# Kernel optimization log

Measured on AMD Instinct MI355X. Metric: run time of the kernel, lower is better.

Reference implementation:

```python
import jax, jax.numpy as jnp
from jax import lax
import numpy as np

B, C, L = 8, 64, 32768
K = 4
DEPTH = 8


def _causal_depthwise_conv(x, weight, dilation):
    # x: [B, C, L], weight: [C, 1, K] depthwise (groups=C). stride=1 so the
    # torch pad formula reduces to left-pad dilation*(K-1), output length L.
    pad = dilation * (K - 1)
    return lax.conv_general_dilated(
        x, weight,
        window_strides=(1,),
        padding=[(pad, 0)],
        rhs_dilation=(dilation,),
        dimension_numbers=("NCH", "OIH", "NCH"),
        feature_group_count=C,
    )


def setup_inputs() -> dict:
    key = jax.random.key(0)
    k1, k2, k3, k4 = jax.random.split(key, 4)
    scalar = np.sqrt(2.0 / (K * 2)).astype(np.float32)
    w_scale = np.sqrt(2.0 / (2 * DEPTH + 4)).astype(np.float32)
    return {
        "x": jax.random.normal(k1, (B, C, L), dtype=jnp.float32),
        "h0": jax.random.uniform(k2, (C, 1, K), minval=-1.0, maxval=1.0, dtype=jnp.float32) * scalar,
        "h1": jax.random.uniform(k3, (C, 1, K), minval=-1.0, maxval=1.0, dtype=jnp.float32) * scalar,
        "w": jax.random.uniform(k4, (C, DEPTH + 2), minval=-1.0, maxval=1.0, dtype=jnp.float32) * w_scale,
    }


def reference(x, h0, h1, w):
    residual_low = x
    y = jnp.zeros_like(x)
    dilation = 1
    for i in range(DEPTH, 0, -1):
        residual_high = _causal_depthwise_conv(residual_low, h1, dilation)
        residual_low = _causal_depthwise_conv(residual_low, h0, dilation)
        y = y + w[:, i][None, :, None] * residual_high
        dilation *= 2
    y = y + w[:, 0][None, :, None] * residual_low
    y = y + x * w[:, -1][None, :, None]
    # dropout p=0 is identity; torch GELU default is exact (erf)
    return jax.nn.gelu(y, approximate=False)
```

## Files before the change

### kernel.cpp

```cpp
#include <hip/hip_runtime.h>
#include <cmath>

namespace {

typedef _Float16 h8 __attribute__((ext_vector_type(8)));

constexpr int C_     = 64;
constexpr int L_     = 32768;
constexpr int TILE   = 4096;
constexpr int HALO   = 776;
constexpr int NB     = TILE + HALO;
constexpr int NU     = NB / 8;
constexpr int HALO_U = HALO / 8;
constexpr int NT     = L_ / TILE;
constexpr int BLK    = 256;
constexpr int UMAX   = (NU + BLK - 1) / BLK;

__device__ __forceinline__ h8 ld8(const _Float16* p) { return *reinterpret_cast<const h8*>(p); }
__device__ __forceinline__ void st8(_Float16* p, h8 v) { *reinterpret_cast<h8*>(p) = v; }
__device__ __forceinline__ float4 ld4f(const float* p) { return *reinterpret_cast<const float4*>(p); }
__device__ __forceinline__ void st4f(float* p, float4 v) { *reinterpret_cast<float4*>(p) = v; }
__device__ __forceinline__ h8 sp8(_Float16 v) { return (h8){v,v,v,v,v,v,v,v}; }

__device__ __forceinline__ h8 fma8(h8 a, h8 b, h8 c) {
    return __builtin_elementwise_fma(a, b, c);
}

template<int K>
__device__ __forceinline__ h8 shconc(h8 A, h8 B) {
    return __builtin_shufflevector(A, B, K, K+1, K+2, K+3, K+4, K+5, K+6, K+7);
}

__device__ __forceinline__ float gelu_f(float v) {
    const float z = v * (1.5957691216057308f + 0.0713548162726f * v * v);
    const float e = __expf(-z);
    return v * __builtin_amdgcn_rcpf(1.0f + e);
}

template<int D, int STARTU, bool LAST>
__device__ __forceinline__ void level_pass(const _Float16* __restrict__ src,
                                           _Float16* __restrict__ dst,
                                           const float* h0f, const float* h1f,
                                           float wi, float w0,
                                           h8* lw, h8* yacc, int tid)
{
    _Float16 c1[4], c0[4];
#pragma unroll
    for (int t = 0; t < 4; ++t) {
        c1[t] = (_Float16)(wi * h1f[t]);
        c0[t] = (_Float16)(LAST ? w0 * h0f[t] : h0f[t]);
    }

#pragma unroll
    for (int u = 0; u < UMAX; ++u) {
        const int un = tid + u * BLK;
        if (un >= STARTU && un < NU) {
            const int p = 8 * un;
            const h8 T3 = lw[u];
            h8 T0, T1, T2;
            if constexpr (D == 1) {
                h8 Lv = ld8(&src[p - 8]);
                T0 = shconc<5>(Lv, T3);
                T1 = shconc<6>(Lv, T3);
                T2 = shconc<7>(Lv, T3);
            } else if constexpr (D == 2) {
                h8 Lv = ld8(&src[p - 8]);
                T0 = shconc<2>(Lv, T3);
                T1 = shconc<4>(Lv, T3);
                T2 = shconc<6>(Lv, T3);
            } else if constexpr (D == 4) {
                h8 Lv  = ld8(&src[p - 8]);
                h8 LL  = ld8(&src[p - 16]);
                T0 = shconc<4>(LL, Lv);
                T1 = Lv;
                T2 = shconc<4>(Lv, T3);
            } else {
                T0 = ld8(&src[p - 3 * D]);
                T1 = ld8(&src[p - 2 * D]);
                T2 = ld8(&src[p - D]);
            }
            if (un >= HALO_U) {
                h8 yv = yacc[u];
                yv = fma8(sp8(c1[0]), T0, yv);
                yv = fma8(sp8(c1[1]), T1, yv);
                yv = fma8(sp8(c1[2]), T2, yv);
                yv = fma8(sp8(c1[3]), T3, yv);
                yacc[u] = yv;
            }
            h8 nl = sp8(c0[0]) * T0;
            nl = fma8(sp8(c0[1]), T1, nl);
            nl = fma8(sp8(c0[2]), T2, nl);
            nl = fma8(sp8(c0[3]), T3, nl);
            if constexpr (LAST) {
                yacc[u] += nl;
            } else {
                lw[u] = nl;
                st8(&dst[p], nl);
            }
        }
    }
}

__global__ __launch_bounds__(BLK, 8)
void cmrc_kernel(const float* __restrict__ x,
                 const float* __restrict__ h0,
                 const float* __restrict__ h1,
                 const float* __restrict__ w,
                 float* __restrict__ out)
{
    __shared__ alignas(16) _Float16 buf[2][NB];

    const int tid  = threadIdx.x;
    const int blk  = blockIdx.x;
    const int tile = blk % NT;
    const int bc   = blk / NT;
    const int c    = bc % C_;
    const long row = (long)bc * L_;
    const int  t0  = tile * TILE - HALO;

    float h0v[4], h1v[4];
#pragma unroll
    for (int k = 0; k < 4; ++k) { h0v[k] = h0[c*4+k]; h1v[k] = h1[c*4+k]; }
    float wv[10];
#pragma unroll
    for (int i = 0; i < 10; ++i) wv[i] = w[c*10+i];

    h8 lw[UMAX];
    h8 yacc[UMAX];

    const _Float16 w9h = (_Float16)wv[9];

#pragma unroll
    for (int u = 0; u < UMAX; ++u) {
        yacc[u] = sp8((_Float16)0.f);
        const int un = tid + u * BLK;
        if (un < NU) {
            const int p = 8 * un;
            const int t = t0 + p;
            float4 xa = make_float4(0.f, 0.f, 0.f, 0.f);
            float4 xb = make_float4(0.f, 0.f, 0.f, 0.f);
            if (t >= 0)     xa = ld4f(&x[row + t]);
            if (t + 4 >= 0) xb = ld4f(&x[row + t + 4]);
            h8 hv;
            hv[0] = (_Float16)xa.x; hv[1] = (_Float16)xa.y;
            hv[2] = (_Float16)xa.z; hv[3] = (_Float16)xa.w;
            hv[4] = (_Float16)xb.x; hv[5] = (_Float16)xb.y;
            hv[6] = (_Float16)xb.z; hv[7] = (_Float16)xb.w;
            st8(&buf[0][p], hv);
            lw[u] = hv;
            if (un >= HALO_U) yacc[u] = sp8(w9h) * hv;
        }
    }
    __syncthreads();

    level_pass<1,   1,  false>(buf[0], buf[1], h0v, h1v, wv[8], 0.f, lw, yacc, tid); __syncthreads();
    level_pass<2,   2,  false>(buf[1], buf[0], h0v, h1v, wv[7], 0.f, lw, yacc, tid); __syncthreads();
    level_pass<4,   4,  false>(buf[0], buf[1], h0v, h1v, wv[6], 0.f, lw, yacc, tid); __syncthreads();
    level_pass<8,   7,  false>(buf[1], buf[0], h0v, h1v, wv[5], 0.f, lw, yacc, tid); __syncthreads();
    level_pass<16,  13, false>(buf[0], buf[1], h0v, h1v, wv[4], 0.f, lw, yacc, tid); __syncthreads();
    level_pass<32,  25, false>(buf[1], buf[0], h0v, h1v, wv[3], 0.f, lw, yacc, tid); __syncthreads();
    level_pass<64,  49, false>(buf[0], buf[1], h0v, h1v, wv[2], 0.f, lw, yacc, tid); __syncthreads();
    level_pass<128, 97, true >(buf[1], buf[0], h0v, h1v, wv[1], wv[0], lw, yacc, tid);

#pragma unroll
    for (int u = 0; u < UMAX; ++u) {
        const int un = tid + u * BLK;
        if (un >= HALO_U && un < NU) {
            const int p = 8 * un;
            const h8 v = yacc[u];
            float4 oa, ob;
            oa.x = gelu_f((float)v[0]); oa.y = gelu_f((float)v[1]);
            oa.z = gelu_f((float)v[2]); oa.w = gelu_f((float)v[3]);
            ob.x = gelu_f((float)v[4]); ob.y = gelu_f((float)v[5]);
            ob.z = gelu_f((float)v[6]); ob.w = gelu_f((float)v[7]);
            st4f(&out[row + t0 + p], oa);
            st4f(&out[row + t0 + p + 4], ob);
        }
    }
}

}

extern "C" void kernel_launch(void* const* d_in, const int* in_sizes, int n_in,
                              void* d_out, int out_size, void* d_ws, size_t ws_size,
                              hipStream_t stream)
{
    const float* x  = (const float*)d_in[0];
    const float* h0 = (const float*)d_in[1];
    const float* h1 = (const float*)d_in[2];
    const float* w  = (const float*)d_in[3];
    float* out = (float*)d_out;

    const int nblocks = (out_size / L_) * NT;
    cmrc_kernel<<<nblocks, BLK, 0, stream>>>(x, h0, h1, w, out);
}
```

Measured before the change: 43.26 us.

## Double tile and block size to cut halo recompute, specialize unit loop, pack via cvt_pkrtz

```diff
diff --git a/kernel.cpp b/kernel.cpp
--- a/kernel.cpp
+++ b/kernel.cpp
@@ -4,17 +4,20 @@
 namespace {
 
 typedef _Float16 h8 __attribute__((ext_vector_type(8)));
+typedef _Float16 h2 __attribute__((ext_vector_type(2)));
+typedef __fp16   fp2 __attribute__((ext_vector_type(2)));
+typedef _Float16 h4 __attribute__((ext_vector_type(4)));
 
 constexpr int C_     = 64;
 constexpr int L_     = 32768;
-constexpr int TILE   = 4096;
+constexpr int TILE   = 8192;
 constexpr int HALO   = 776;
 constexpr int NB     = TILE + HALO;
 constexpr int NU     = NB / 8;
 constexpr int HALO_U = HALO / 8;
 constexpr int NT     = L_ / TILE;
-constexpr int BLK    = 256;
-constexpr int UMAX   = (NU + BLK - 1) / BLK;
+constexpr int BLK    = 512;
+constexpr int S2N    = NU - 2 * BLK;
 
 __device__ __forceinline__ h8 ld8(const _Float16* p) { return *reinterpret_cast<const h8*>(p); }
 __device__ __forceinline__ void st8(_Float16* p, h8 v) { *reinterpret_cast<h8*>(p) = v; }
@@ -31,10 +34,60 @@
     return __builtin_shufflevector(A, B, K, K+1, K+2, K+3, K+4, K+5, K+6, K+7);
 }
 
+__device__ __forceinline__ h2 pkrtz(float lo, float hi) {
+    const fp2 r = __builtin_amdgcn_cvt_pkrtz(lo, hi);
+    return __builtin_bit_cast(h2, r);
+}
+__device__ __forceinline__ h8 pack8(float4 a, float4 b) {
+    const h2 p0 = pkrtz(a.x, a.y);
+    const h2 p1 = pkrtz(a.z, a.w);
+    const h2 p2 = pkrtz(b.x, b.y);
+    const h2 p3 = pkrtz(b.z, b.w);
+    return (h8){p0[0], p0[1], p1[0], p1[1], p2[0], p2[1], p3[0], p3[1]};
+}
+
 __device__ __forceinline__ float gelu_f(float v) {
     const float z = v * (1.5957691216057308f + 0.0713548162726f * v * v);
     const float e = __expf(-z);
     return v * __builtin_amdgcn_rcpf(1.0f + e);
+}
+
+template<int D, bool LAST>
+__device__ __forceinline__ void unit_math(const _Float16* __restrict__ src,
+                                          int p, h8& lwv, h8& yv, bool doY,
+                                          const _Float16* c1, const _Float16* c0)
+{
+    const h8 T3 = lwv;
+    h8 T0, T1, T2;
+    if constexpr (D == 1) {
+        const h8 Lv = ld8(&src[p - 8]);
+        T0 = shconc<5>(Lv, T3); T1 = shconc<6>(Lv, T3); T2 = shconc<7>(Lv, T3);
+    } else if constexpr (D == 2) {
+        const h8 Lv = ld8(&src[p - 8]);
+        T0 = shconc<2>(Lv, T3); T1 = shconc<4>(Lv, T3); T2 = shconc<6>(Lv, T3);
+    } else if constexpr (D == 4) {
+        const h8 Lv = ld8(&src[p - 8]);
+        const h8 LL = ld8(&src[p - 16]);
+        T0 = shconc<4>(LL, Lv); T1 = Lv; T2 = shconc<4>(Lv, T3);
+    } else {
+        T0 = ld8(&src[p - 3 * D]);
+        T1 = ld8(&src[p - 2 * D]);
+        T2 = ld8(&src[p - D]);
+    }
+    if (doY) {
+        h8 yt = yv;
+        yt = fma8(sp8(c1[0]), T0, yt);
+        yt = fma8(sp8(c1[1]), T1, yt);
+        yt = fma8(sp8(c1[2]), T2, yt);
+        yt = fma8(sp8(c1[3]), T3, yt);
+        yv = yt;
+    }
+    h8 nl = sp8(c0[0]) * T0;
+    nl = fma8(sp8(c0[1]), T1, nl);
+    nl = fma8(sp8(c0[2]), T2, nl);
+    nl = fma8(sp8(c0[3]), T3, nl);
+    if constexpr (LAST) yv += nl;
+    else lwv = nl;
 }
 
 template<int D, int STARTU, bool LAST>
@@ -50,54 +103,17 @@
         c1[t] = (_Float16)(wi * h1f[t]);
         c0[t] = (_Float16)(LAST ? w0 * h0f[t] : h0f[t]);
     }
-
-#pragma unroll
-    for (int u = 0; u < UMAX; ++u) {
-        const int un = tid + u * BLK;
-        if (un >= STARTU && un < NU) {
-            const int p = 8 * un;
-            const h8 T3 = lw[u];
-            h8 T0, T1, T2;
-            if constexpr (D == 1) {
-                h8 Lv = ld8(&src[p - 8]);
-                T0 = shconc<5>(Lv, T3);
-                T1 = shconc<6>(Lv, T3);
-                T2 = shconc<7>(Lv, T3);
-            } else if constexpr (D == 2) {
-                h8 Lv = ld8(&src[p - 8]);
-                T0 = shconc<2>(Lv, T3);
-                T1 = shconc<4>(Lv, T3);
-                T2 = shconc<6>(Lv, T3);
-            } else if constexpr (D == 4) {
-                h8 Lv  = ld8(&src[p - 8]);
-                h8 LL  = ld8(&src[p - 16]);
-                T0 = shconc<4>(LL, Lv);
-                T1 = Lv;
-                T2 = shconc<4>(Lv, T3);
-            } else {
-                T0 = ld8(&src[p - 3 * D]);
-                T1 = ld8(&src[p - 2 * D]);
-                T2 = ld8(&src[p - D]);
-            }
-            if (un >= HALO_U) {
-                h8 yv = yacc[u];
-                yv = fma8(sp8(c1[0]), T0, yv);
-                yv = fma8(sp8(c1[1]), T1, yv);
-                yv = fma8(sp8(c1[2]), T2, yv);
-                yv = fma8(sp8(c1[3]), T3, yv);
-                yacc[u] = yv;
-            }
-            h8 nl = sp8(c0[0]) * T0;
-            nl = fma8(sp8(c0[1]), T1, nl);
-            nl = fma8(sp8(c0[2]), T2, nl);
-            nl = fma8(sp8(c0[3]), T3, nl);
-            if constexpr (LAST) {
-                yacc[u] += nl;
-            } else {
-                lw[u] = nl;
-                st8(&dst[p], nl);
-            }
-        }
+    if (tid >= STARTU) {
+        unit_math<D, LAST>(src, 8 * tid, lw[0], yacc[0], tid >= HALO_U, c1, c0);
+        if constexpr (!LAST) st8(&dst[8 * tid], lw[0]);
+    }
+    {
+        unit_math<D, LAST>(src, 8 * (tid + BLK), lw[1], yacc[1], true, c1, c0);
+        if constexpr (!LAST) st8(&dst[8 * (tid + BLK)], lw[1]);
+    }
+    if (tid < S2N) {
+        unit_math<D, LAST>(src, 8 * (tid + 2 * BLK), lw[2], yacc[2], true, c1, c0);
+        if constexpr (!LAST) st8(&dst[8 * (tid + 2 * BLK)], lw[2]);
     }
 }
 
@@ -125,31 +141,33 @@
 #pragma unroll
     for (int i = 0; i < 10; ++i) wv[i] = w[c*10+i];
 
-    h8 lw[UMAX];
-    h8 yacc[UMAX];
+    h8 lw[3];
+    h8 yacc[3];
 
     const _Float16 w9h = (_Float16)wv[9];
 
-#pragma unroll
-    for (int u = 0; u < UMAX; ++u) {
-        yacc[u] = sp8((_Float16)0.f);
-        const int un = tid + u * BLK;
-        if (un < NU) {
-            const int p = 8 * un;
-            const int t = t0 + p;
-            float4 xa = make_float4(0.f, 0.f, 0.f, 0.f);
-            float4 xb = make_float4(0.f, 0.f, 0.f, 0.f);
-            if (t >= 0)     xa = ld4f(&x[row + t]);
-            if (t + 4 >= 0) xb = ld4f(&x[row + t + 4]);
-            h8 hv;
-            hv[0] = (_Float16)xa.x; hv[1] = (_Float16)xa.y;
-            hv[2] = (_Float16)xa.z; hv[3] = (_Float16)xa.w;
-            hv[4] = (_Float16)xb.x; hv[5] = (_Float16)xb.y;
-            hv[6] = (_Float16)xb.z; hv[7] = (_Float16)xb.w;
-            st8(&buf[0][p], hv);
-            lw[u] = hv;
-            if (un >= HALO_U) yacc[u] = sp8(w9h) * hv;
-        }
+    {
+        const int t = t0 + 8 * tid;
+        float4 xa = make_float4(0.f,0.f,0.f,0.f), xb = xa;
+        if (t >= 0) { xa = ld4f(&x[row + t]); xb = ld4f(&x[row + t + 4]); }
+        const h8 hv = pack8(xa, xb);
+        st8(&buf[0][8 * tid], hv);
+        lw[0] = hv;
+        yacc[0] = sp8(w9h) * hv;
+    }
+    {
+        const int t = t0 + 8 * (tid + BLK);
+        const h8 hv = pack8(ld4f(&x[row + t]), ld4f(&x[row + t + 4]));
+        st8(&buf[0][8 * (tid + BLK)], hv);
+        lw[1] = hv;
+        yacc[1] = sp8(w9h) * hv;
+    }
+    if (tid < S2N) {
+        const int t = t0 + 8 * (tid + 2 * BLK);
+        const h8 hv = pack8(ld4f(&x[row + t]), ld4f(&x[row + t + 4]));
+        st8(&buf[0][8 * (tid + 2 * BLK)], hv);
+        lw[2] = hv;
+        yacc[2] = sp8(w9h) * hv;
     }
     __syncthreads();
 
@@ -162,21 +180,19 @@
     level_pass<64,  49, false>(buf[0], buf[1], h0v, h1v, wv[2], 0.f, lw, yacc, tid); __syncthreads();
     level_pass<128, 97, true >(buf[1], buf[0], h0v, h1v, wv[1], wv[0], lw, yacc, tid);
 
-#pragma unroll
-    for (int u = 0; u < UMAX; ++u) {
-        const int un = tid + u * BLK;
-        if (un >= HALO_U && un < NU) {
-            const int p = 8 * un;
-            const h8 v = yacc[u];
-            float4 oa, ob;
-            oa.x = gelu_f((float)v[0]); oa.y = gelu_f((float)v[1]);
-            oa.z = gelu_f((float)v[2]); oa.w = gelu_f((float)v[3]);
-            ob.x = gelu_f((float)v[4]); ob.y = gelu_f((float)v[5]);
-            ob.z = gelu_f((float)v[6]); ob.w = gelu_f((float)v[7]);
-            st4f(&out[row + t0 + p], oa);
-            st4f(&out[row + t0 + p + 4], ob);
-        }
-    }
+    auto emit = [&](int un, h8 v) {
+        float4 oa, ob;
+        oa.x = gelu_f((float)v[0]); oa.y = gelu_f((float)v[1]);
+        oa.z = gelu_f((float)v[2]); oa.w = gelu_f((float)v[3]);
+        ob.x = gelu_f((float)v[4]); ob.y = gelu_f((float)v[5]);
+        ob.z = gelu_f((float)v[6]); ob.w = gelu_f((float)v[7]);
+        const long idx = row + (t0 + 8 * un);
+        st4f(&out[idx], oa);
+        st4f(&out[idx + 4], ob);
+    };
+    if (tid >= HALO_U) emit(tid, yacc[0]);
+    emit(tid + BLK, yacc[1]);
+    if (tid < S2N) emit(tid + 2 * BLK, yacc[2]);
 }
 
 }
```

Measured after the change: 45.55 us. +5.3%, slower.
